# Optimization experiments

Measured on AMD Instinct MI355X. Metric: run time of the kernel, lower is better.

Reference implementation:

```python
import jax, jax.numpy as jnp
import numpy as np

EPS = 1e-4

def softmax_kernel(data, proj, is_query):
    # FAVOR+ positive softmax random features; data: [b,h,l,d], proj: [d,m]
    d = data.shape[-1]
    m = proj.shape[-1]
    data_normalizer = d ** -0.25  # normalize_data=True
    ratio = m ** -0.5
    data_dash = jnp.einsum('bhld,dm->bhlm', data, proj) * data_normalizer
    diag = 0.5 * jnp.sum(data * data, axis=-1, keepdims=True) * (data_normalizer ** 2)
    if is_query:
        stab = jnp.max(data_dash, axis=-1, keepdims=True)   # per-token max
    else:
        stab = jnp.max(data_dash, axis=(-2, -1), keepdims=True)  # per (b,h) max
    out = ratio * (jnp.exp(data_dash - diag - stab) + EPS)
    return out, stab

def low_mem_attn(qp, kp, v, causal, chunk):
    # qp,kp: [b,h,l,m] positive features; v: [b,h,l,d]
    b, h, l, m = qp.shape
    d = v.shape[-1]
    if not causal:
        kv = jnp.einsum('bhlm,bhld->bhmd', kp, v)
        den = jnp.einsum('bhlm,bhm->bhl', qp, jnp.sum(kp, axis=2))
        return jnp.einsum('bhlm,bhmd->bhld', qp, kv) / den[..., None]
    nc = l // chunk
    qc = qp.reshape(b, h, nc, chunk, m)
    kc = kp.reshape(b, h, nc, chunk, m)
    vc = v.reshape(b, h, nc, chunk, d)
    # intra-chunk causal part
    mask = jnp.tril(jnp.ones((chunk, chunk), dtype=qp.dtype))
    scores = jnp.einsum('bhcim,bhcjm->bhcij', qc, kc) * mask
    intra = jnp.einsum('bhcij,bhcjd->bhcid', scores, vc)
    intra_den = jnp.sum(scores, axis=-1)  # [b,h,nc,chunk]
    # inter-chunk via exclusive cumulative sums of KV state
    kv = jnp.einsum('bhcjm,bhcjd->bhcmd', kc, vc)          # per-chunk KV
    kv_prev = jnp.cumsum(kv, axis=2) - kv                   # exclusive cumsum
    ks = jnp.sum(kc, axis=3)                                # [b,h,nc,m]
    ks_prev = jnp.cumsum(ks, axis=2) - ks
    inter = jnp.einsum('bhcim,bhcmd->bhcid', qc, kv_prev)
    inter_den = jnp.einsum('bhcim,bhcm->bhci', qc, ks_prev)
    out = (intra + inter) / (intra_den + inter_den)[..., None]
    return out.reshape(b, h, l, d)


def setup_inputs() -> dict:
    key = jax.random.key(0)
    k1, k2, k3, k4 = jax.random.split(key, 4)
    B, H, L, D, M = 2, 16, 4096, 64, 64
    return {
        'q': jax.random.normal(k1, (B, H, L, D), dtype=jnp.float32),
        'k': jax.random.normal(k2, (B, H, L, D), dtype=jnp.float32),
        'v': jax.random.normal(k3, (B, H, L, D), dtype=jnp.float32),
        'projection_matrix': jax.random.normal(k4, (D, M), dtype=jnp.float32),
        'chunk_size': 128,
    }


def reference(q, k, v, projection_matrix, chunk_size):
    qp, _ = softmax_kernel(q, projection_matrix, is_query=True)
    kp, _key_maxima = softmax_kernel(k, projection_matrix, is_query=False)
    o = low_mem_attn(qp, kp, v, causal=True, chunk=chunk_size)
    return o
```

## Files before the change

### kernel.cpp

```cpp
#include <hip/hip_runtime.h>
#include <hip/hip_bf16.h>

#define TPB 256
#define ATPB 512

constexpr int   Bc = 2, Hc = 16, Lc = 4096, Dc = 64, Mc = 64, CHc = 128;
constexpr int   NCc = Lc / CHc;
constexpr int   BHc = Bc * Hc;
constexpr float DNF    = 0.35355339059327373f;
constexpr float RATIOF = 0.125f;
constexpr float EPSF   = 1e-4f;

constexpr long QP_OFF  = 0;
constexpr long KPB_OFF = 4194304;
constexpr long KV_OFF  = 8388608;
constexpr long KVB_OFF = 12582912;
constexpr long KS_OFF  = 14680064;
constexpr long HM_OFF  = 14745600;

typedef __attribute__((ext_vector_type(8))) short bf16x8;
typedef __attribute__((ext_vector_type(4))) float f32x4;

__device__ __forceinline__ unsigned fordmap(float f) {
  unsigned u = __float_as_uint(f);
  return (u & 0x80000000u) ? ~u : (u | 0x80000000u);
}
__device__ __forceinline__ float fordunmap(unsigned u) {
  return __uint_as_float((u & 0x80000000u) ? (u & 0x7fffffffu) : ~u);
}
__device__ __forceinline__ unsigned pk2(float a, float b) {
  union { __hip_bfloat16 h; unsigned short u; } ca, cb;
  ca.h = __float2bfloat16(a); cb.h = __float2bfloat16(b);
  return ((unsigned)cb.u << 16) | (unsigned)ca.u;
}
__device__ __forceinline__ short f2bf(float a) {
  union { __hip_bfloat16 h; short s; } c; c.h = __float2bfloat16(a); return c.s;
}
__device__ __forceinline__ float bf2f(short s) {
  return __uint_as_float(((unsigned)(unsigned short)s) << 16);
}
__device__ __forceinline__ bf16x8 ldfrag(const float* __restrict__ p) {
  const float4 lo = *(const float4*)p;
  const float4 hi = *(const float4*)(p + 4);
  bf16x8 a;
  unsigned* u = (unsigned*)&a;
  u[0] = pk2(lo.x, lo.y); u[1] = pk2(lo.z, lo.w);
  u[2] = pk2(hi.x, hi.y); u[3] = pk2(hi.z, hi.w);
  return a;
}

__global__ __launch_bounds__(TPB) void k_fs(const float* __restrict__ q,
                                            const float* __restrict__ kin,
                                            const float* __restrict__ P,
                                            short* __restrict__ qpb,
                                            unsigned* __restrict__ hmax) {
  __shared__ short Pt[64 * 72];
  __shared__ short ob[128 * 64];
  __shared__ float diag_s[128];
  __shared__ unsigned bmax_s;
  const int t = threadIdx.x;
  const bool isq = blockIdx.x < 1024;
  const int cb = isq ? blockIdx.x : (blockIdx.x - 1024);
  const float* __restrict__ x = isq ? q : kin;
  const long rowbase = (long)cb * 128;
  for (int i = t; i < 4096; i += TPB) {
    const int d = i >> 6, m = i & 63;
    Pt[m * 72 + d] = f2bf(P[i]);
  }
  if (t == 0) bmax_s = 0u;
  if (isq) {
    const int row = t >> 1, half = t & 1;
    float s = 0.f;
#pragma unroll
    for (int d = 0; d < 32; d += 4) {
      float4 vv = *(const float4*)&x[(rowbase + row) * 64 + half * 32 + d];
      s += vv.x * vv.x + vv.y * vv.y + vv.z * vv.z + vv.w * vv.w;
    }
    s += __shfl_xor(s, 1);
    if (half == 0) diag_s[row] = 0.0625f * s;
  }
  __syncthreads();

  const int w = t >> 6, lane = t & 63;
  const int lrow = lane & 15, quad = lane >> 4;
  float tmax = -1e30f;
#pragma unroll
  for (int rt2 = 0; rt2 < 2; ++rt2) {
    const int rt = w * 2 + rt2;
    const float* xr = &x[(rowbase + rt * 16 + lrow) * 64];
    const bf16x8 a0 = ldfrag(xr + quad * 8);
    const bf16x8 a1 = ldfrag(xr + 32 + quad * 8);
    f32x4 c[4];
#pragma unroll
    for (int ct = 0; ct < 4; ++ct) {
      const bf16x8 b0 = *(const bf16x8*)&Pt[(ct * 16 + lrow) * 72 + quad * 8];
      const bf16x8 b1 = *(const bf16x8*)&Pt[(ct * 16 + lrow) * 72 + 32 + quad * 8];
      f32x4 cc = {0.f, 0.f, 0.f, 0.f};
      cc = __builtin_amdgcn_mfma_f32_16x16x32_bf16(a0, b0, cc, 0, 0, 0);
      cc = __builtin_amdgcn_mfma_f32_16x16x32_bf16(a1, b1, cc, 0, 0, 0);
#pragma unroll
      for (int r = 0; r < 4; ++r) cc[r] *= DNF;
      c[ct] = cc;
    }
    if (isq) {
#pragma unroll
      for (int r = 0; r < 4; ++r) {
        float mx = fmaxf(fmaxf(c[0][r], c[1][r]), fmaxf(c[2][r], c[3][r]));
#pragma unroll
        for (int off = 1; off < 16; off <<= 1) mx = fmaxf(mx, __shfl_xor(mx, off));
        const int row = rt * 16 + quad * 4 + r;
        const float dg = diag_s[row];
#pragma unroll
        for (int ct = 0; ct < 4; ++ct)
          ob[row * 64 + ct * 16 + lrow] =
              f2bf(RATIOF * (expf(c[ct][r] - dg - mx) + EPSF));
      }
    } else {
#pragma unroll
      for (int ct = 0; ct < 4; ++ct)
#pragma unroll
        for (int r = 0; r < 4; ++r) tmax = fmaxf(tmax, c[ct][r]);
    }
  }
  if (!isq) {
#pragma unroll
    for (int off = 1; off < 64; off <<= 1) tmax = fmaxf(tmax, __shfl_xor(tmax, off));
    if (lane == 0) atomicMax(&bmax_s, fordmap(tmax));
  }
  __syncthreads();
  if (isq) {
    for (int i = t; i < 1024; i += TPB)
      *(uint4*)&qpb[rowbase * 64 + i * 8] = *(const uint4*)&ob[i * 8];
  } else {
    if (t == 0) atomicMax(&hmax[cb >> 5], bmax_s);
  }
}

__global__ __launch_bounds__(TPB) void k_kv(const float* __restrict__ kin,
                                            const float* __restrict__ v,
                                            const float* __restrict__ P,
                                            float* __restrict__ kvT,
                                            float* __restrict__ ks,
                                            short* __restrict__ kpb,
                                            const unsigned* __restrict__ hmax) {
  __shared__ short Pt[64 * 72];
  __shared__ short Kt[64 * 136];
  __shared__ short Vt[64 * 136];
  __shared__ float diag_s[128];
  __shared__ float ks_s[64];
  const int t = threadIdx.x;
  const int bhc = blockIdx.x;
  const long base = (long)bhc * 8192;
  const float stab = fordunmap(hmax[bhc >> 5]);
  if (t < 64) ks_s[t] = 0.f;
  for (int i = t; i < 4096; i += TPB) {
    const int d = i >> 6, m = i & 63;
    Pt[m * 72 + d] = f2bf(P[i]);
  }
  {
    const int d2 = (t & 31) * 2;
    for (int i = t; i < 4096; i += TPB) {
      const int j = i >> 5;
      float2 vv = *(const float2*)&v[base + j * 64 + d2];
      Vt[d2 * 136 + j] = f2bf(vv.x);
      Vt[(d2 + 1) * 136 + j] = f2bf(vv.y);
    }
  }
  {
    const int row = t >> 1, half = t & 1;
    float s = 0.f;
#pragma unroll
    for (int d = 0; d < 32; d += 4) {
      float4 vv = *(const float4*)&kin[base + row * 64 + half * 32 + d];
      s += vv.x * vv.x + vv.y * vv.y + vv.z * vv.z + vv.w * vv.w;
    }
    s += __shfl_xor(s, 1);
    if (half == 0) diag_s[row] = 0.0625f * s;
  }
  __syncthreads();
  const int w = t >> 6, lane = t & 63;
  const int lrow = lane & 15, quad = lane >> 4;
  float ksp_[4] = {0.f, 0.f, 0.f, 0.f};
#pragma unroll
  for (int rt2 = 0; rt2 < 2; ++rt2) {
    const int rt = w * 2 + rt2;
    const float* kr = &kin[base + (rt * 16 + lrow) * 64];
    const bf16x8 a0 = ldfrag(kr + quad * 8);
    const bf16x8 a1 = ldfrag(kr + 32 + quad * 8);
#pragma unroll
    for (int ct = 0; ct < 4; ++ct) {
      const bf16x8 b0 = *(const bf16x8*)&Pt[(ct * 16 + lrow) * 72 + quad * 8];
      const bf16x8 b1 = *(const bf16x8*)&Pt[(ct * 16 + lrow) * 72 + 32 + quad * 8];
      f32x4 cc = {0.f, 0.f, 0.f, 0.f};
      cc = __builtin_amdgcn_mfma_f32_16x16x32_bf16(a0, b0, cc, 0, 0, 0);
      cc = __builtin_amdgcn_mfma_f32_16x16x32_bf16(a1, b1, cc, 0, 0, 0);
      const int m = ct * 16 + lrow;
#pragma unroll
      for (int r = 0; r < 4; ++r) {
        const int row = rt * 16 + quad * 4 + r;
        const float e = RATIOF * (expf(cc[r] * DNF - diag_s[row] - stab) + EPSF);
        Kt[m * 136 + row] = f2bf(e);
        ksp_[ct] += e;
      }
    }
  }
#pragma unroll
  for (int ct = 0; ct < 4; ++ct) {
    ksp_[ct] += __shfl_xor(ksp_[ct], 16);
    ksp_[ct] += __shfl_xor(ksp_[ct], 32);
  }
  if (quad == 0) {
#pragma unroll
    for (int ct = 0; ct < 4; ++ct) atomicAdd(&ks_s[ct * 16 + lrow], ksp_[ct]);
  }
  __syncthreads();
  if (t < 64) ks[bhc * 64 + t] = ks_s[t];
  for (int i = t; i < 1024; i += TPB) {
    const int j = i >> 3, m8 = (i & 7) * 8;
    unsigned u[4];
#pragma unroll
    for (int p = 0; p < 4; ++p) {
      const unsigned lo = (unsigned short)Kt[(m8 + 2 * p) * 136 + j];
      const unsigned hi = (unsigned short)Kt[(m8 + 2 * p + 1) * 136 + j];
      u[p] = lo | (hi << 16);
    }
    uint4 w4; w4.x = u[0]; w4.y = u[1]; w4.z = u[2]; w4.w = u[3];
    *(uint4*)&kpb[base + j * 64 + m8] = w4;
  }
  f32x4 acc[4];
#pragma unroll
  for (int mt = 0; mt < 4; ++mt) acc[mt] = (f32x4){0.f, 0.f, 0.f, 0.f};
#pragma unroll
  for (int ksq = 0; ksq < 4; ++ksq) {
    const bf16x8 a = *(const bf16x8*)&Vt[(w * 16 + lrow) * 136 + ksq * 32 + quad * 8];
#pragma unroll
    for (int mt = 0; mt < 4; ++mt) {
      const bf16x8 b = *(const bf16x8*)&Kt[(mt * 16 + lrow) * 136 + ksq * 32 + quad * 8];
      acc[mt] = __builtin_amdgcn_mfma_f32_16x16x32_bf16(a, b, acc[mt], 0, 0, 0);
    }
  }
  const long kvo = (long)bhc * 4096;
#pragma unroll
  for (int mt = 0; mt < 4; ++mt)
#pragma unroll
    for (int r = 0; r < 4; ++r)
      kvT[kvo + (long)(w * 16 + quad * 4 + r) * 64 + mt * 16 + lrow] = acc[mt][r];
}

__global__ void k_scan(const float* __restrict__ kv, short* __restrict__ kvb,
                       float* __restrict__ ks) {
  if (blockIdx.x < 512) {
    const int tid = blockIdx.x * TPB + threadIdx.x;
    const int bh = tid >> 12, rem = tid & 4095;
    float run = 0.f;
    for (int c = 0; c < NCc; ++c) {
      const long idx = ((long)(bh * NCc + c)) * 4096 + rem;
      kvb[idx] = f2bf(run);
      run += kv[idx];
    }
  } else {
    for (int tid = threadIdx.x; tid < BHc * 64; tid += TPB) {
      const int bh = tid >> 6, m = tid & 63;
      float run = 0.f;
      for (int c = 0; c < NCc; ++c) {
        const int idx = (bh * NCc + c) * 64 + m;
        const float val = ks[idx];
        ks[idx] = run;
        run += val;
      }
    }
  }
}

__global__ __launch_bounds__(ATPB, 4) void k_attn(const short* __restrict__ qpb,
                                                  const short* __restrict__ kpb,
                                                  const float* __restrict__ v,
                                                  const short* __restrict__ kvb,
                                                  const float* __restrict__ ksp,
                                                  float* __restrict__ outp) {
  __shared__ short Ks[128 * 72];
  __shared__ short Vt[64 * 136];
  __shared__ short KVt[64 * 72];
  __shared__ short Ps[128 * 136];
  __shared__ float kss[64];
  __shared__ float dens[128];
  const int t = threadIdx.x;
  const int bhc = blockIdx.x;
  const long cbase = (long)bhc * 8192;

  for (int i = t; i < 1024; i += ATPB) {
    const int r = i >> 3, c8 = (i & 7) * 8;
    *(uint4*)&Ks[r * 72 + c8] = *(const uint4*)&kpb[cbase + r * 64 + c8];
  }
  for (int i = t; i < 4096; i += ATPB) {
    const int jp = i >> 6, d = i & 63;
    const float a = v[cbase + (2 * jp) * 64 + d];
    const float b = v[cbase + (2 * jp + 1) * 64 + d];
    *(unsigned*)&Vt[d * 136 + 2 * jp] = pk2(a, b);
  }
  {
    const int d = t >> 3, c8 = (t & 7) * 8;
    *(uint4*)&KVt[d * 72 + c8] = *(const uint4*)&kvb[(long)bhc * 4096 + d * 64 + c8];
  }
  if (t < 64) kss[t] = ksp[bhc * 64 + t];
  for (int i = t; i < 1024; i += ATPB) {
    const int tp = i >> 8, rr = (i >> 4) & 15, cc = i & 15;
    Ps[(tp * 32 + rr) * 136 + tp * 32 + 16 + cc] = 0;
  }
  const int w = t >> 6, lane = t & 63;
  const int lrow = lane & 15, quad = lane >> 4;
  const int ri = w;
  const long qrb = cbase + (long)(ri * 16 + lrow) * 64;
  const bf16x8 a0 = *(const bf16x8*)&qpb[qrb + quad * 8];
  const bf16x8 a1 = *(const bf16x8*)&qpb[qrb + 32 + quad * 8];
  __syncthreads();

  float qks = 0.f;
#pragma unroll
  for (int j = 0; j < 8; ++j) {
    qks += bf2f(a0[j]) * kss[quad * 8 + j];
    qks += bf2f(a1[j]) * kss[32 + quad * 8 + j];
  }
  qks += __shfl_xor(qks, 16);
  qks += __shfl_xor(qks, 32);
  if (quad == 0) dens[ri * 16 + lrow] = qks;

  float rs0 = 0.f, rs1 = 0.f, rs2 = 0.f, rs3 = 0.f;
  for (int cj = 0; cj <= ri; ++cj) {
    const bf16x8 b0 = *(const bf16x8*)&Ks[(cj * 16 + lrow) * 72 + quad * 8];
    const bf16x8 b1 = *(const bf16x8*)&Ks[(cj * 16 + lrow) * 72 + 32 + quad * 8];
    f32x4 c = {0.f, 0.f, 0.f, 0.f};
    c = __builtin_amdgcn_mfma_f32_16x16x32_bf16(a0, b0, c, 0, 0, 0);
    c = __builtin_amdgcn_mfma_f32_16x16x32_bf16(a1, b1, c, 0, 0, 0);
    if (cj == ri) {
#pragma unroll
      for (int r = 0; r < 4; ++r)
        if (lrow > quad * 4 + r) c[r] = 0.f;
    }
    const int colb = cj * 16 + lrow;
    Ps[(ri * 16 + quad * 4 + 0) * 136 + colb] = f2bf(c[0]); rs0 += c[0];
    Ps[(ri * 16 + quad * 4 + 1) * 136 + colb] = f2bf(c[1]); rs1 += c[1];
    Ps[(ri * 16 + quad * 4 + 2) * 136 + colb] = f2bf(c[2]); rs2 += c[2];
    Ps[(ri * 16 + quad * 4 + 3) * 136 + colb] = f2bf(c[3]); rs3 += c[3];
  }
#pragma unroll
  for (int off = 1; off < 16; off <<= 1) {
    rs0 += __shfl_xor(rs0, off);
    rs1 += __shfl_xor(rs1, off);
    rs2 += __shfl_xor(rs2, off);
    rs3 += __shfl_xor(rs3, off);
  }
  if (lrow == 0) {
    dens[ri * 16 + quad * 4 + 0] += rs0;
    dens[ri * 16 + quad * 4 + 1] += rs1;
    dens[ri * 16 + quad * 4 + 2] += rs2;
    dens[ri * 16 + quad * 4 + 3] += rs3;
  }

  f32x4 acc0 = {0.f,0.f,0.f,0.f}, acc1 = {0.f,0.f,0.f,0.f};
  f32x4 acc2 = {0.f,0.f,0.f,0.f}, acc3 = {0.f,0.f,0.f,0.f};
  const int nj = (ri + 2) >> 1;
  for (int jc = 0; jc < nj; ++jc) {
    const bf16x8 a  = *(const bf16x8*)&Ps[(ri * 16 + lrow) * 136 + jc * 32 + quad * 8];
    const bf16x8 b0 = *(const bf16x8*)&Vt[(lrow) * 136 + jc * 32 + quad * 8];
    const bf16x8 b1 = *(const bf16x8*)&Vt[(16 + lrow) * 136 + jc * 32 + quad * 8];
    const bf16x8 b2 = *(const bf16x8*)&Vt[(32 + lrow) * 136 + jc * 32 + quad * 8];
    const bf16x8 b3 = *(const bf16x8*)&Vt[(48 + lrow) * 136 + jc * 32 + quad * 8];
    acc0 = __builtin_amdgcn_mfma_f32_16x16x32_bf16(a, b0, acc0, 0, 0, 0);
    acc1 = __builtin_amdgcn_mfma_f32_16x16x32_bf16(a, b1, acc1, 0, 0, 0);
    acc2 = __builtin_amdgcn_mfma_f32_16x16x32_bf16(a, b2, acc2, 0, 0, 0);
    acc3 = __builtin_amdgcn_mfma_f32_16x16x32_bf16(a, b3, acc3, 0, 0, 0);
  }
  {
    const bf16x8 b0 = *(const bf16x8*)&KVt[(lrow) * 72 + quad * 8];
    const bf16x8 b1 = *(const bf16x8*)&KVt[(16 + lrow) * 72 + quad * 8];
    const bf16x8 b2 = *(const bf16x8*)&KVt[(32 + lrow) * 72 + quad * 8];
    const bf16x8 b3 = *(const bf16x8*)&KVt[(48 + lrow) * 72 + quad * 8];
    acc0 = __builtin_amdgcn_mfma_f32_16x16x32_bf16(a0, b0, acc0, 0, 0, 0);
    acc1 = __builtin_amdgcn_mfma_f32_16x16x32_bf16(a0, b1, acc1, 0, 0, 0);
    acc2 = __builtin_amdgcn_mfma_f32_16x16x32_bf16(a0, b2, acc2, 0, 0, 0);
    acc3 = __builtin_amdgcn_mfma_f32_16x16x32_bf16(a0, b3, acc3, 0, 0, 0);
    const bf16x8 c0 = *(const bf16x8*)&KVt[(lrow) * 72 + 32 + quad * 8];
    const bf16x8 c1 = *(const bf16x8*)&KVt[(16 + lrow) * 72 + 32 + quad * 8];
    const bf16x8 c2 = *(const bf16x8*)&KVt[(32 + lrow) * 72 + 32 + quad * 8];
    const bf16x8 c3 = *(const bf16x8*)&KVt[(48 + lrow) * 72 + 32 + quad * 8];
    acc0 = __builtin_amdgcn_mfma_f32_16x16x32_bf16(a1, c0, acc0, 0, 0, 0);
    acc1 = __builtin_amdgcn_mfma_f32_16x16x32_bf16(a1, c1, acc1, 0, 0, 0);
    acc2 = __builtin_amdgcn_mfma_f32_16x16x32_bf16(a1, c2, acc2, 0, 0, 0);
    acc3 = __builtin_amdgcn_mfma_f32_16x16x32_bf16(a1, c3, acc3, 0, 0, 0);
  }
#pragma unroll
  for (int r = 0; r < 4; ++r) {
    const int row = ri * 16 + quad * 4 + r;
    const float inv = 1.f / dens[row];
    const long ob = cbase + (long)row * 64 + lrow;
    outp[ob]      = acc0[r] * inv;
    outp[ob + 16] = acc1[r] * inv;
    outp[ob + 32] = acc2[r] * inv;
    outp[ob + 48] = acc3[r] * inv;
  }
}

extern "C" void kernel_launch(void* const* d_in, const int* in_sizes, int n_in,
                              void* d_out, int out_size, void* d_ws, size_t ws_size,
                              hipStream_t stream) {
  const float* q = (const float*)d_in[0];
  const float* k = (const float*)d_in[1];
  const float* v = (const float*)d_in[2];
  const float* P = (const float*)d_in[3];
  float* ws = (float*)d_ws;
  short*    qpb  = (short*)(ws + QP_OFF);
  short*    kpb  = (short*)(ws + KPB_OFF);
  float*    kvT  = ws + KV_OFF;
  short*    kvb  = (short*)(ws + KVB_OFF);
  float*    ks   = ws + KS_OFF;
  unsigned* hmax = (unsigned*)(ws + HM_OFF);
  float* out = (float*)d_out;

  hipMemsetAsync(hmax, 0, BHc * sizeof(unsigned), stream);
  k_fs<<<dim3(2048), dim3(TPB), 0, stream>>>(q, k, P, qpb, hmax);
  k_kv<<<dim3(1024), dim3(TPB), 0, stream>>>(k, v, P, kvT, ks, kpb, hmax);
  k_scan<<<dim3(513), dim3(TPB), 0, stream>>>(kvT, kvb, ks);
  k_attn<<<dim3(1024), dim3(ATPB), 0, stream>>>(qpb, kpb, v, kvb, ks, out);
}
```

Before: 195.1 us.

## Fuse exclusive KV prefix scan into attention kernel, drop scan launch

Removes the separate k_scan kernel. Each attention block now sums the per-chunk KV states and key sums of all earlier chunks itself, reading fp32 kvT directly and converting to bf16 in shared memory. This saves one kernel launch and the bf16 kvb write and read round-trip. In exchange, later chunks redundantly read up to 31 previous 16KB KV blocks, so total reads grow roughly quadratically per head and the load is unbalanced across blocks, though these reads are likely L2-resident.

After: 210.6 us. 7.9% more time.

```diff
diff --git a/kernel.cpp b/kernel.cpp
--- a/kernel.cpp
+++ b/kernel.cpp
@@ -14,9 +14,8 @@
 constexpr long QP_OFF  = 0;
 constexpr long KPB_OFF = 4194304;
 constexpr long KV_OFF  = 8388608;
-constexpr long KVB_OFF = 12582912;
-constexpr long KS_OFF  = 14680064;
-constexpr long HM_OFF  = 14745600;
+constexpr long KS_OFF  = 12582912;
+constexpr long HM_OFF  = 12648448;
 
 typedef __attribute__((ext_vector_type(8))) short bf16x8;
 typedef __attribute__((ext_vector_type(4))) float f32x4;
@@ -247,35 +246,10 @@
       kvT[kvo + (long)(w * 16 + quad * 4 + r) * 64 + mt * 16 + lrow] = acc[mt][r];
 }
 
-__global__ void k_scan(const float* __restrict__ kv, short* __restrict__ kvb,
-                       float* __restrict__ ks) {
-  if (blockIdx.x < 512) {
-    const int tid = blockIdx.x * TPB + threadIdx.x;
-    const int bh = tid >> 12, rem = tid & 4095;
-    float run = 0.f;
-    for (int c = 0; c < NCc; ++c) {
-      const long idx = ((long)(bh * NCc + c)) * 4096 + rem;
-      kvb[idx] = f2bf(run);
-      run += kv[idx];
-    }
-  } else {
-    for (int tid = threadIdx.x; tid < BHc * 64; tid += TPB) {
-      const int bh = tid >> 6, m = tid & 63;
-      float run = 0.f;
-      for (int c = 0; c < NCc; ++c) {
-        const int idx = (bh * NCc + c) * 64 + m;
-        const float val = ks[idx];
-        ks[idx] = run;
-        run += val;
-      }
-    }
-  }
-}
-
 __global__ __launch_bounds__(ATPB, 4) void k_attn(const short* __restrict__ qpb,
                                                   const short* __restrict__ kpb,
                                                   const float* __restrict__ v,
-                                                  const short* __restrict__ kvb,
+                                                  const float* __restrict__ kvT,
                                                   const float* __restrict__ ksp,
                                                   float* __restrict__ outp) {
   __shared__ short Ks[128 * 72];
@@ -286,6 +260,7 @@
   __shared__ float dens[128];
   const int t = threadIdx.x;
   const int bhc = blockIdx.x;
+  const int bh = bhc >> 5, cb = bhc & 31;
   const long cbase = (long)bhc * 8192;
 
   for (int i = t; i < 1024; i += ATPB) {
@@ -299,10 +274,26 @@
     *(unsigned*)&Vt[d * 136 + 2 * jp] = pk2(a, b);
   }
   {
-    const int d = t >> 3, c8 = (t & 7) * 8;
-    *(uint4*)&KVt[d * 72 + c8] = *(const uint4*)&kvb[(long)bhc * 4096 + d * 64 + c8];
-  }
-  if (t < 64) kss[t] = ksp[bhc * 64 + t];
+    const int flat = t * 8;
+    const int d = flat >> 6, m = flat & 63;
+    float run[8] = {0.f, 0.f, 0.f, 0.f, 0.f, 0.f, 0.f, 0.f};
+    const float* kvp = &kvT[(long)(bh * NCc) * 4096 + flat];
+    for (int c = 0; c < cb; ++c) {
+      const float4 lo = *(const float4*)&kvp[(long)c * 4096];
+      const float4 hi = *(const float4*)&kvp[(long)c * 4096 + 4];
+      run[0] += lo.x; run[1] += lo.y; run[2] += lo.z; run[3] += lo.w;
+      run[4] += hi.x; run[5] += hi.y; run[6] += hi.z; run[7] += hi.w;
+    }
+    short* kt = &KVt[d * 72 + m];
+#pragma unroll
+    for (int j = 0; j < 8; ++j) kt[j] = f2bf(run[j]);
+  }
+  if (t < 64) {
+    float run = 0.f;
+    const float* kp_ = &ksp[(bh * NCc) * 64 + t];
+    for (int c = 0; c < cb; ++c) run += kp_[c * 64];
+    kss[t] = run;
+  }
   for (int i = t; i < 1024; i += ATPB) {
     const int tp = i >> 8, rr = (i >> 4) & 15, cc = i & 15;
     Ps[(tp * 32 + rr) * 136 + tp * 32 + 16 + cc] = 0;
@@ -412,7 +403,6 @@
   short*    qpb  = (short*)(ws + QP_OFF);
   short*    kpb  = (short*)(ws + KPB_OFF);
   float*    kvT  = ws + KV_OFF;
-  short*    kvb  = (short*)(ws + KVB_OFF);
   float*    ks   = ws + KS_OFF;
   unsigned* hmax = (unsigned*)(ws + HM_OFF);
   float* out = (float*)d_out;
@@ -420,6 +410,5 @@
   hipMemsetAsync(hmax, 0, BHc * sizeof(unsigned), stream);
   k_fs<<<dim3(2048), dim3(TPB), 0, stream>>>(q, k, P, qpb, hmax);
   k_kv<<<dim3(1024), dim3(TPB), 0, stream>>>(k, v, P, kvT, ks, kpb, hmax);
-  k_scan<<<dim3(513), dim3(TPB), 0, stream>>>(kvT, kvb, ks);
-  k_attn<<<dim3(1024), dim3(ATPB), 0, stream>>>(qpb, kpb, v, kvb, ks, out);
-}
+  k_attn<<<dim3(1024), dim3(ATPB), 0, stream>>>(qpb, kpb, v, kvT, ks, out);
+}
```
